# Optimization experiments

Measured on AMD Instinct MI355X. Metric: run time of the kernel, lower is better.

The kernel has to match this reference:

```python
import jax, jax.numpy as jnp
import numpy as np

B, S, H = 32, 2048, 1024

def setup_inputs() -> dict:
    key = jax.random.key(0)
    k1, k2, k3, k4 = jax.random.split(key, 4)
    encoded_states = jax.random.normal(k1, (B, S, H), dtype=jnp.float32)
    # exactly one formula token (label 2) per sample at position 0.
    raw = jax.random.randint(k2, (B, S), 0, 10)
    sr_label = jnp.where(raw < 2, raw, -100)
    sr_label = sr_label.at[:, 0].set(2)
    W1 = jax.random.normal(k3, (H, 2 * H), dtype=jnp.float32) * (1.0 / np.sqrt(2 * H))
    b1 = jnp.zeros((H,), dtype=jnp.float32)
    W2 = jax.random.normal(k4, (2, H), dtype=jnp.float32) * (1.0 / np.sqrt(H))
    b2 = jnp.zeros((2,), dtype=jnp.float32)
    return {"encoded_states": encoded_states, "sr_label": sr_label,
            "W1": W1, "b1": b1, "W2": W2, "b2": b2}

def reference(encoded_states, sr_label, W1, b1, W2, b2):
    dt = encoded_states.dtype
    header_mask = (sr_label >= 0) & (sr_label < 2)          # (b, s)
    formula_mask = (sr_label == 2).astype(dt)               # exactly one per row
    # gather the single formula embedding per sample via masked sum
    formula_emb = jnp.einsum('bs,bsh->bh', formula_mask, encoded_states)  # (b, h)
    fuse = jnp.concatenate(
        [encoded_states, jnp.broadcast_to(formula_emb[:, None, :], encoded_states.shape)],
        axis=-1)                                             # (b, s, 2h)
    hid = jax.nn.gelu(jnp.einsum('bsf,hf->bsh', fuse, W1) + b1, approximate=False)
    logits = jnp.einsum('bsh,ch->bsc', hid, W2) + b2         # (b, s, 2)
    logp = jax.nn.log_softmax(logits, axis=-1)
    labels = jnp.clip(sr_label, 0, 1)                        # safe index; masked below
    tok_loss = -jnp.take_along_axis(logp, labels[..., None], axis=-1)[..., 0]
    m = header_mask.astype(dt)
    cnt = m.sum(axis=1)                                      # valid headers per sample
    sample_loss = (tok_loss * m).sum(axis=1) / jnp.maximum(cnt, 1.0)  # CE mean per sample
    valid = (cnt > 0).astype(dt)
    loss = (sample_loss * valid).sum() / (valid.sum() + 1e-6)
    return loss, logits, header_mask
```

## Files before the change

### kernel.cpp

```cpp
#include <hip/hip_runtime.h>
#include <math.h>


typedef __bf16 bf16x8 __attribute__((ext_vector_type(8)));
typedef float f32x4 __attribute__((ext_vector_type(4)));

struct alignas(16) BF8 { __bf16 h[8]; };
struct alignas(8)  BF4 { __bf16 h[4]; };

typedef const __attribute__((address_space(1))) void glb_void;
typedef __attribute__((address_space(3))) void lds_void;

#define SEQ 2048
#define NB  32
#define HID 1024
#define MROWS (NB * SEQ)
#define NKT 16

__device__ __forceinline__ float gelu_bf(float x) {
    float z  = 0.70710678118f * x;
    float az = fabsf(z);
    float t  = __builtin_amdgcn_rcpf(fmaf(0.3275911f, az, 1.0f));
    float poly = fmaf(fmaf(fmaf(fmaf(1.061405429f, t, -1.453152027f), t,
                         1.421413741f), t, -0.284496736f), t, 0.254829592f) * t;
    float ex = __expf(-az * az);
    float er = copysignf(fmaf(-poly, ex, 1.0f), z);
    return 0.5f * x * (1.0f + er);
}

__global__ void sr_init_logits(float* __restrict__ logits, const float* __restrict__ b2) {
    int i = blockIdx.x * 256 + threadIdx.x;
    if (i < MROWS * 2) logits[i] = b2[i & 1];
}

__global__ void sr_conv_w1(const float* __restrict__ W1, __bf16* __restrict__ Bt) {
    int gid = blockIdx.x * 256 + threadIdx.x;
    int h = gid >> 8;
    int kb = (gid & 255) * 4;
    float4 v = *(const float4*)&W1[(size_t)h * 2048 + kb];
    BF4 o;
    o.h[0] = (__bf16)v.x; o.h[1] = (__bf16)v.y; o.h[2] = (__bf16)v.z; o.h[3] = (__bf16)v.w;
    *(BF4*)&Bt[(size_t)h * 1024 + kb] = o;
}

__global__ void sr_femb(const float* __restrict__ enc, const int* __restrict__ lab,
                        float* __restrict__ femb) {
    __shared__ int cnt;
    __shared__ int idl[64];
    int b = blockIdx.x;
    int tid = threadIdx.x;
    if (tid == 0) cnt = 0;
    __syncthreads();
    for (int s = tid; s < SEQ; s += 256)
        if (lab[b * SEQ + s] == 2) {
            int p = atomicAdd(&cnt, 1);
            if (p < 64) idl[p] = s;
        }
    __syncthreads();
    float4 a = {0.f, 0.f, 0.f, 0.f};
    int n = cnt < 64 ? cnt : 64;
    for (int i = 0; i < n; ++i) {
        float4 v = *(const float4*)&enc[((size_t)b * SEQ + idl[i]) * HID + tid * 4];
        a.x += v.x; a.y += v.y; a.z += v.z; a.w += v.w;
    }
    *(float4*)&femb[b * HID + tid * 4] = a;
}

__global__ void sr_fc(const float* __restrict__ femb, const float* __restrict__ W1,
                      const float* __restrict__ b1, float* __restrict__ fcout) {
    int gw = (blockIdx.x * 256 + threadIdx.x) >> 6;
    int lane = threadIdx.x & 63;
    for (int i = 0; i < 16; ++i) {
        int d = gw * 16 + i;
        int b = d >> 10, h = d & 1023;
        const float* fe = femb + b * HID;
        const float* wr = W1 + (size_t)h * 2048 + 1024;
        float p = 0.f;
        #pragma unroll
        for (int t = 0; t < 16; ++t) {
            int k = lane + t * 64;
            p += fe[k] * wr[k];
        }
        #pragma unroll
        for (int off = 32; off; off >>= 1) p += __shfl_down(p, off);
        if (lane == 0) fcout[d] = p + b1[h];
    }
}

__global__ __launch_bounds__(512, 2)
void sr_gemm11(const float* __restrict__ enc, const __bf16* __restrict__ Bt,
               const float* __restrict__ fc, const float* __restrict__ W2,
               float* __restrict__ partg) {
    __shared__ __align__(16) unsigned char smem[139264];
    __bf16* LAb = (__bf16*)smem;
    __bf16* LBb = (__bf16*)(smem + 65536);
    float*  red = (float*)smem;

    int bid = blockIdx.x;
    int lgc = (bid & 7) * 128 + (bid >> 3);
    int pm = lgc >> 2, pn = lgc & 3;
    const int row0 = pm * 256, col0 = pn * 256;

    int tid = threadIdx.x;
    int wid = tid >> 6, lane = tid & 63;
    int wr = wid >> 2, wc = wid & 3;
    int l15 = lane & 15, lq = lane >> 4;

    f32x4 acc[2][2][4][2] = {};
    float4 fa[4][2];

    #define LOAD_A(kt) do {                                                       \
        _Pragma("unroll")                                                         \
        for (int i = 0; i < 4; ++i) {                                             \
            int q = i * 512 + tid;                                                \
            int r = q >> 3, c = q & 7;                                            \
            int sc = (c ^ (r & 7)) * 8 + (kt) * 64;                               \
            const float* s0 = &enc[(size_t)(row0 + r) * HID + sc];                \
            fa[i][0] = *(const float4*)s0;                                        \
            fa[i][1] = *(const float4*)(s0 + 4);                                  \
        }                                                                         \
    } while (0)

    #define WRITE_A(buf) do {                                                     \
        _Pragma("unroll")                                                         \
        for (int i = 0; i < 4; ++i) {                                             \
            int q = i * 512 + tid;                                                \
            BF8 t;                                                                \
            t.h[0] = (__bf16)fa[i][0].x; t.h[1] = (__bf16)fa[i][0].y;             \
            t.h[2] = (__bf16)fa[i][0].z; t.h[3] = (__bf16)fa[i][0].w;             \
            t.h[4] = (__bf16)fa[i][1].x; t.h[5] = (__bf16)fa[i][1].y;             \
            t.h[6] = (__bf16)fa[i][1].z; t.h[7] = (__bf16)fa[i][1].w;             \
            *(BF8*)&LAb[(buf) * 16384 + q * 8] = t;                               \
        }                                                                         \
    } while (0)

    #define STAGE_B(buf, kt) do {                                                 \
        _Pragma("unroll")                                                         \
        for (int i = 0; i < 4; ++i) {                                             \
            int q = i * 512 + tid;                                                \
            int r = q >> 3, c = q & 7;                                            \
            int sc = (c ^ (r & 7)) * 8 + (kt) * 64;                               \
            __builtin_amdgcn_global_load_lds(                                     \
                (glb_void*)(Bt + (size_t)(col0 + r) * HID + sc),                  \
                (lds_void*)(LBb + (buf) * 16384 + q * 8), 16, 0, 0);              \
        }                                                                         \
    } while (0)

    LOAD_A(0);
    STAGE_B(0, 0);
    WRITE_A(0);
    __syncthreads();

    int cur = 0;
    for (int kt = 0; kt < NKT; ++kt) {
        if (kt + 1 < NKT) {
            LOAD_A(kt + 1);
            STAGE_B(cur ^ 1, kt + 1);
        }

        const __bf16* LAc = LAb + cur * 16384;
        const __bf16* LBc = LBb + cur * 16384;
        bf16x8 bfr[2][2][2];
        #pragma unroll
        for (int qb = 0; qb < 2; ++qb)
            #pragma unroll
            for (int n = 0; n < 2; ++n)
                #pragma unroll
                for (int kk = 0; kk < 2; ++kk) {
                    int r = qb * 128 + wc * 32 + n * 16 + l15;
                    bfr[qb][n][kk] = *(const bf16x8*)
                        &LBc[r * 64 + (((kk * 4 + lq) ^ (r & 7)) * 8)];
                }
        #pragma unroll
        for (int qa = 0; qa < 2; ++qa) {
            bf16x8 af[4][2];
            #pragma unroll
            for (int m = 0; m < 4; ++m)
                #pragma unroll
                for (int kk = 0; kk < 2; ++kk) {
                    int r = qa * 128 + wr * 64 + m * 16 + l15;
                    af[m][kk] = *(const bf16x8*)
                        &LAc[r * 64 + (((kk * 4 + lq) ^ (r & 7)) * 8)];
                }
            #pragma unroll
            for (int qb = 0; qb < 2; ++qb)
                #pragma unroll
                for (int m = 0; m < 4; ++m)
                    #pragma unroll
                    for (int n = 0; n < 2; ++n)
                        #pragma unroll
                        for (int kk = 0; kk < 2; ++kk)
                            acc[qa][qb][m][n] = __builtin_amdgcn_mfma_f32_16x16x32_bf16(
                                af[m][kk], bfr[qb][n][kk], acc[qa][qb][m][n], 0, 0, 0);
        }

        if (kt + 1 < NKT) WRITE_A(cur ^ 1);
        __syncthreads();
        cur ^= 1;
    }
    #undef LOAD_A
    #undef WRITE_A
    #undef STAGE_B

    int b = row0 >> 11;
    float fcv[2][2], w2a[2][2], w2b[2][2];
    #pragma unroll
    for (int qb = 0; qb < 2; ++qb)
        #pragma unroll
        for (int n = 0; n < 2; ++n) {
            int h = col0 + qb * 128 + wc * 32 + n * 16 + l15;
            fcv[qb][n] = fc[b * HID + h];
            w2a[qb][n] = W2[h];
            w2b[qb][n] = W2[HID + h];
        }
    int e = wc * 16 + l15;
    #pragma unroll
    for (int qa = 0; qa < 2; ++qa)
        #pragma unroll
        for (int m = 0; m < 4; ++m)
            #pragma unroll
            for (int j = 0; j < 4; ++j) {
                int rloc = qa * 128 + wr * 64 + m * 16 + lq * 4 + j;
                float p0 = 0.f, p1 = 0.f;
                #pragma unroll
                for (int qb = 0; qb < 2; ++qb)
                    #pragma unroll
                    for (int n = 0; n < 2; ++n) {
                        float g = gelu_bf(acc[qa][qb][m][n][j] + fcv[qb][n]);
                        p0 += g * w2a[qb][n];
                        p1 += g * w2b[qb][n];
                    }
                red[(rloc * 2 + 0) * 68 + e] = p0;
                red[(rloc * 2 + 1) * 68 + e] = p1;
            }
    __syncthreads();
    {
        const f32x4* rp = (const f32x4*)&red[tid * 68];
        f32x4 sv = {0.f, 0.f, 0.f, 0.f};
        #pragma unroll
        for (int i = 0; i < 16; ++i) sv += rp[i];
        float s = sv[0] + sv[1] + sv[2] + sv[3];
        int row = tid >> 1, c = tid & 1;
        partg[((size_t)pn * MROWS + row0 + row) * 2 + c] = s;
    }
}

__global__ __launch_bounds__(256, 2)
void sr_gemm_fused(const float* __restrict__ enc, const __bf16* __restrict__ Bt,
                   const float* __restrict__ fc, const float* __restrict__ W2,
                   float* __restrict__ logits) {
    __shared__ __bf16 As[128 * 64];
    __shared__ __bf16 Bs[128 * 64];

    int bid = blockIdx.x;
    int logical = (bid & 7) * 512 + (bid >> 3);
    int pm = logical >> 3;
    int pn = logical & 7;

    int tid = threadIdx.x;
    int wid = tid >> 6, lane = tid & 63;
    int wm = wid >> 1, wn = wid & 1;

    const int row0 = pm * 128;
    const int col0 = pn * 128;

    f32x4 acc[4][4] = {};

    for (int kt = 0; kt < 16; ++kt) {
        int k0 = kt * 64;
        #pragma unroll
        for (int i = 0; i < 4; ++i) {
            int q = i * 256 + tid;
            int r = q >> 3;
            int cb = (q & 7) * 8;
            const __bf16* src = Bt + (size_t)(col0 + r) * 1024 + k0 + cb;
            __builtin_amdgcn_global_load_lds((glb_void*)src, (lds_void*)&Bs[q * 8], 16, 0, 0);
        }
        #pragma unroll
        for (int pp = 0; pp < 4; ++pp) {
            int e = pp * 2048 + tid * 8;
            int r = e >> 6, c = e & 63;
            const float* src = enc + (size_t)(row0 + r) * 1024 + k0 + c;
            float4 f0 = *(const float4*)src;
            float4 f1 = *(const float4*)(src + 4);
            BF8 t;
            t.h[0] = (__bf16)f0.x; t.h[1] = (__bf16)f0.y;
            t.h[2] = (__bf16)f0.z; t.h[3] = (__bf16)f0.w;
            t.h[4] = (__bf16)f1.x; t.h[5] = (__bf16)f1.y;
            t.h[6] = (__bf16)f1.z; t.h[7] = (__bf16)f1.w;
            *(BF8*)&As[r * 64 + c] = t;
        }
        __syncthreads();
        int lrow = lane & 15;
        int ak = (lane >> 4) * 8;
        #pragma unroll
        for (int kk = 0; kk < 2; ++kk) {
            bf16x8 a[4], b[4];
            #pragma unroll
            for (int m = 0; m < 4; ++m)
                a[m] = *(const bf16x8*)&As[(wm * 64 + m * 16 + lrow) * 64 + kk * 32 + ak];
            #pragma unroll
            for (int n = 0; n < 4; ++n)
                b[n] = *(const bf16x8*)&Bs[(wn * 64 + n * 16 + lrow) * 64 + kk * 32 + ak];
            #pragma unroll
            for (int m = 0; m < 4; ++m)
                #pragma unroll
                for (int n = 0; n < 4; ++n)
                    acc[m][n] = __builtin_amdgcn_mfma_f32_16x16x32_bf16(a[m], b[n], acc[m][n], 0, 0, 0);
        }
        __syncthreads();
    }

    int bidx = row0 >> 11;
    float fcv[4], w2a[4], w2b[4];
    #pragma unroll
    for (int n = 0; n < 4; ++n) {
        int h = col0 + wn * 64 + n * 16 + (lane & 15);
        fcv[n] = fc[bidx * HID + h];
        w2a[n] = W2[h];
        w2b[n] = W2[HID + h];
    }
    #pragma unroll
    for (int m = 0; m < 4; ++m) {
        int rbase = row0 + wm * 64 + m * 16 + (lane >> 4) * 4;
        #pragma unroll
        for (int j = 0; j < 4; ++j) {
            float p0 = 0.f, p1 = 0.f;
            #pragma unroll
            for (int n = 0; n < 4; ++n) {
                float g = gelu_bf(acc[m][n][j] + fcv[n]);
                p0 += g * w2a[n];
                p1 += g * w2b[n];
            }
            #pragma unroll
            for (int off = 1; off < 16; off <<= 1) {
                p0 += __shfl_xor(p0, off);
                p1 += __shfl_xor(p1, off);
            }
            if ((lane & 15) == 0) {
                int rg = rbase + j;
                atomicAdd(&logits[rg * 2 + 0], p0);
                atomicAdd(&logits[rg * 2 + 1], p1);
            }
        }
    }
}

__global__ void sr_loss_pg(const int* __restrict__ lab, const float* __restrict__ partg,
                           const float* __restrict__ b2, float* __restrict__ logits,
                           float* __restrict__ mask_out, float* __restrict__ sl,
                           float* __restrict__ validv) {
    int b = blockIdx.x;
    int tid = threadIdx.x;
    float b20 = b2[0], b21 = b2[1];
    float lsum = 0.f; int lcnt = 0;
    for (int s = tid; s < SEQ; s += 256) {
        size_t row = (size_t)b * SEQ + s;
        float l0 = b20, l1 = b21;
        #pragma unroll
        for (int q = 0; q < 4; ++q) {
            l0 += partg[((size_t)q * MROWS + row) * 2 + 0];
            l1 += partg[((size_t)q * MROWS + row) * 2 + 1];
        }
        logits[row * 2 + 0] = l0;
        logits[row * 2 + 1] = l1;
        int l = lab[row];
        bool hdr = (l == 0) || (l == 1);
        mask_out[row] = hdr ? 1.0f : 0.0f;
        if (hdr) {
            float mx = fmaxf(l0, l1);
            float lse = mx + logf(expf(l0 - mx) + expf(l1 - mx));
            lsum += lse - (l == 0 ? l0 : l1);
            lcnt++;
        }
    }
    #pragma unroll
    for (int off = 32; off; off >>= 1) {
        lsum += __shfl_down(lsum, off);
        lcnt += __shfl_down(lcnt, off);
    }
    __shared__ float wsum[4];
    __shared__ int wcnt[4];
    int wid = tid >> 6, lane = tid & 63;
    if (lane == 0) { wsum[wid] = lsum; wcnt[wid] = lcnt; }
    __syncthreads();
    if (tid == 0) {
        float S = wsum[0] + wsum[1] + wsum[2] + wsum[3];
        int C = wcnt[0] + wcnt[1] + wcnt[2] + wcnt[3];
        sl[b] = (C > 0) ? S / (float)C : 0.0f;
        validv[b] = (C > 0) ? 1.0f : 0.0f;
    }
}

__global__ void sr_loss(const int* __restrict__ lab, const float* __restrict__ logits,
                        float* __restrict__ mask_out, float* __restrict__ sl,
                        float* __restrict__ validv) {
    int b = blockIdx.x;
    int tid = threadIdx.x;
    float lsum = 0.f; int lcnt = 0;
    for (int s = tid; s < SEQ; s += 256) {
        int l = lab[b * SEQ + s];
        bool hdr = (l == 0) || (l == 1);
        mask_out[b * SEQ + s] = hdr ? 1.0f : 0.0f;
        if (hdr) {
            float l0 = logits[(b * SEQ + s) * 2];
            float l1 = logits[(b * SEQ + s) * 2 + 1];
            float mx = fmaxf(l0, l1);
            float lse = mx + logf(expf(l0 - mx) + expf(l1 - mx));
            lsum += lse - (l == 0 ? l0 : l1);
            lcnt++;
        }
    }
    #pragma unroll
    for (int off = 32; off; off >>= 1) {
        lsum += __shfl_down(lsum, off);
        lcnt += __shfl_down(lcnt, off);
    }
    __shared__ float wsum[4];
    __shared__ int wcnt[4];
    int wid = tid >> 6, lane = tid & 63;
    if (lane == 0) { wsum[wid] = lsum; wcnt[wid] = lcnt; }
    __syncthreads();
    if (tid == 0) {
        float S = wsum[0] + wsum[1] + wsum[2] + wsum[3];
        int C = wcnt[0] + wcnt[1] + wcnt[2] + wcnt[3];
        sl[b] = (C > 0) ? S / (float)C : 0.0f;
        validv[b] = (C > 0) ? 1.0f : 0.0f;
    }
}

__global__ void sr_final(const float* __restrict__ sl, const float* __restrict__ validv,
                         float* __restrict__ out) {
    if (threadIdx.x == 0) {
        float s = 0.f, v = 0.f;
        for (int b = 0; b < NB; ++b) { s += sl[b]; v += validv[b]; }
        out[0] = s / (v + 1e-6f);
    }
}

extern "C" void kernel_launch(void* const* d_in, const int* in_sizes, int n_in,
                              void* d_out, int out_size, void* d_ws, size_t ws_size,
                              hipStream_t stream) {
    const float* enc = (const float*)d_in[0];
    const int*   lab = (const int*)d_in[1];
    const float* W1  = (const float*)d_in[2];
    const float* b1  = (const float*)d_in[3];
    const float* W2  = (const float*)d_in[4];
    const float* b2  = (const float*)d_in[5];

    float* out     = (float*)d_out;
    float* loss    = out;
    float* logits  = out + 1;
    float* maskout = out + 1 + MROWS * 2;

    float* ws     = (float*)d_ws;
    float* femb   = ws;
    float* fc     = ws + 32768;
    float* sl     = ws + 65536;
    float* validv = ws + 65568;
    float* partg  = ws + 65600;
    __bf16* Bt    = (__bf16*)(ws + 65600 + 2 * 524288);

    const size_t need = (65600u + 2u * 524288u) * 4u + (size_t)HID * HID * 2u;

    sr_conv_w1<<<1024, 256, 0, stream>>>(W1, Bt);
    sr_femb<<<32, 256, 0, stream>>>(enc, lab, femb);
    sr_fc<<<512, 256, 0, stream>>>(femb, W1, b1, fc);

    if (ws_size >= need) {
        sr_gemm11<<<1024, 512, 0, stream>>>(enc, Bt, fc, W2, partg);
        sr_loss_pg<<<32, 256, 0, stream>>>(lab, partg, b2, logits, maskout, sl, validv);
    } else {
        sr_init_logits<<<512, 256, 0, stream>>>(logits, b2);
        sr_gemm_fused<<<4096, 256, 0, stream>>>(enc, Bt, fc, W2, logits);
        sr_loss<<<32, 256, 0, stream>>>(lab, logits, maskout, sl, validv);
    }

    sr_final<<<1, 64, 0, stream>>>(sl, validv, loss);
}
```

Baseline: 263.2 us.

## Load A fragments directly to registers, giving each wave full tile width

The GEMM kernel no longer stages the fp32 activation tile through LDS as bf16. Each wave now loads its own 32 rows of A straight from global memory into registers, converts them to bf16 in place, and computes against all 256 columns of the B tile held in LDS. This removes the A shared-memory writes and reads and cuts LDS use from about 136KB to 64KB. In exchange each wave reads 16 B fragments from LDS per k-step with less reuse, and the A global loads use a less coalesced row-per-lane pattern. The cross-wave reduction buffer also shrinks.

Measured after the change: 279.6 us. 6.2% more time.

```diff
diff --git a/kernel.cpp b/kernel.cpp
--- a/kernel.cpp
+++ b/kernel.cpp
@@ -88,12 +88,11 @@
 }
 
 __global__ __launch_bounds__(512, 2)
-void sr_gemm11(const float* __restrict__ enc, const __bf16* __restrict__ Bt,
+void sr_gemm15(const float* __restrict__ enc, const __bf16* __restrict__ Bt,
                const float* __restrict__ fc, const float* __restrict__ W2,
                float* __restrict__ partg) {
-    __shared__ __align__(16) unsigned char smem[139264];
-    __bf16* LAb = (__bf16*)smem;
-    __bf16* LBb = (__bf16*)(smem + 65536);
+    __shared__ __align__(16) unsigned char smem[65536];
+    __bf16* LBb = (__bf16*)smem;
     float*  red = (float*)smem;
 
     int bid = blockIdx.x;
@@ -103,35 +102,40 @@
 
     int tid = threadIdx.x;
     int wid = tid >> 6, lane = tid & 63;
-    int wr = wid >> 2, wc = wid & 3;
     int l15 = lane & 15, lq = lane >> 4;
 
-    f32x4 acc[2][2][4][2] = {};
-    float4 fa[4][2];
+    f32x4 acc[2][16] = {};
+    float4 a32[2][2][2];
+    bf16x8 afb[2][2];
+
+    const float* arow0 = enc + (size_t)(row0 + wid * 32 + l15) * HID + lq * 8;
+    const float* arow1 = arow0 + 16 * HID;
 
     #define LOAD_A(kt) do {                                                       \
+        const float* s0 = arow0 + (kt) * 64;                                      \
+        const float* s1 = arow1 + (kt) * 64;                                      \
+        a32[0][0][0] = *(const float4*)s0;                                        \
+        a32[0][0][1] = *(const float4*)(s0 + 4);                                  \
+        a32[0][1][0] = *(const float4*)(s0 + 32);                                 \
+        a32[0][1][1] = *(const float4*)(s0 + 36);                                 \
+        a32[1][0][0] = *(const float4*)s1;                                        \
+        a32[1][0][1] = *(const float4*)(s1 + 4);                                  \
+        a32[1][1][0] = *(const float4*)(s1 + 32);                                 \
+        a32[1][1][1] = *(const float4*)(s1 + 36);                                 \
+    } while (0)
+
+    #define CVT_A() do {                                                          \
         _Pragma("unroll")                                                         \
-        for (int i = 0; i < 4; ++i) {                                             \
-            int q = i * 512 + tid;                                                \
-            int r = q >> 3, c = q & 7;                                            \
-            int sc = (c ^ (r & 7)) * 8 + (kt) * 64;                               \
-            const float* s0 = &enc[(size_t)(row0 + r) * HID + sc];                \
-            fa[i][0] = *(const float4*)s0;                                        \
-            fa[i][1] = *(const float4*)(s0 + 4);                                  \
-        }                                                                         \
-    } while (0)
-
-    #define WRITE_A(buf) do {                                                     \
-        _Pragma("unroll")                                                         \
-        for (int i = 0; i < 4; ++i) {                                             \
-            int q = i * 512 + tid;                                                \
-            BF8 t;                                                                \
-            t.h[0] = (__bf16)fa[i][0].x; t.h[1] = (__bf16)fa[i][0].y;             \
-            t.h[2] = (__bf16)fa[i][0].z; t.h[3] = (__bf16)fa[i][0].w;             \
-            t.h[4] = (__bf16)fa[i][1].x; t.h[5] = (__bf16)fa[i][1].y;             \
-            t.h[6] = (__bf16)fa[i][1].z; t.h[7] = (__bf16)fa[i][1].w;             \
-            *(BF8*)&LAb[(buf) * 16384 + q * 8] = t;                               \
-        }                                                                         \
+        for (int m = 0; m < 2; ++m)                                               \
+            _Pragma("unroll")                                                     \
+            for (int kk = 0; kk < 2; ++kk) {                                      \
+                BF8 t;                                                            \
+                t.h[0] = (__bf16)a32[m][kk][0].x; t.h[1] = (__bf16)a32[m][kk][0].y;\
+                t.h[2] = (__bf16)a32[m][kk][0].z; t.h[3] = (__bf16)a32[m][kk][0].w;\
+                t.h[4] = (__bf16)a32[m][kk][1].x; t.h[5] = (__bf16)a32[m][kk][1].y;\
+                t.h[6] = (__bf16)a32[m][kk][1].z; t.h[7] = (__bf16)a32[m][kk][1].w;\
+                afb[m][kk] = *(bf16x8*)&t;                                        \
+            }                                                                     \
     } while (0)
 
     #define STAGE_B(buf, kt) do {                                                 \
@@ -148,97 +152,64 @@
 
     LOAD_A(0);
     STAGE_B(0, 0);
-    WRITE_A(0);
     __syncthreads();
 
     int cur = 0;
     for (int kt = 0; kt < NKT; ++kt) {
-        if (kt + 1 < NKT) {
-            LOAD_A(kt + 1);
-            STAGE_B(cur ^ 1, kt + 1);
-        }
-
-        const __bf16* LAc = LAb + cur * 16384;
+        CVT_A();
+        int ktn = (kt + 1 < NKT) ? kt + 1 : NKT - 1;
+        LOAD_A(ktn);
+        if (kt + 1 < NKT) STAGE_B(cur ^ 1, kt + 1);
+
         const __bf16* LBc = LBb + cur * 16384;
-        bf16x8 bfr[2][2][2];
-        #pragma unroll
-        for (int qb = 0; qb < 2; ++qb)
-            #pragma unroll
-            for (int n = 0; n < 2; ++n)
-                #pragma unroll
-                for (int kk = 0; kk < 2; ++kk) {
-                    int r = qb * 128 + wc * 32 + n * 16 + l15;
-                    bfr[qb][n][kk] = *(const bf16x8*)
-                        &LBc[r * 64 + (((kk * 4 + lq) ^ (r & 7)) * 8)];
-                }
-        #pragma unroll
-        for (int qa = 0; qa < 2; ++qa) {
-            bf16x8 af[4][2];
-            #pragma unroll
-            for (int m = 0; m < 4; ++m)
-                #pragma unroll
-                for (int kk = 0; kk < 2; ++kk) {
-                    int r = qa * 128 + wr * 64 + m * 16 + l15;
-                    af[m][kk] = *(const bf16x8*)
-                        &LAc[r * 64 + (((kk * 4 + lq) ^ (r & 7)) * 8)];
-                }
-            #pragma unroll
-            for (int qb = 0; qb < 2; ++qb)
-                #pragma unroll
-                for (int m = 0; m < 4; ++m)
-                    #pragma unroll
-                    for (int n = 0; n < 2; ++n)
-                        #pragma unroll
-                        for (int kk = 0; kk < 2; ++kk)
-                            acc[qa][qb][m][n] = __builtin_amdgcn_mfma_f32_16x16x32_bf16(
-                                af[m][kk], bfr[qb][n][kk], acc[qa][qb][m][n], 0, 0, 0);
-        }
-
-        if (kt + 1 < NKT) WRITE_A(cur ^ 1);
+        #pragma unroll
+        for (int n = 0; n < 16; ++n) {
+            int r = n * 16 + l15;
+            bf16x8 b0 = *(const bf16x8*)&LBc[r * 64 + ((lq ^ (r & 7)) * 8)];
+            bf16x8 b1 = *(const bf16x8*)&LBc[r * 64 + (((4 + lq) ^ (r & 7)) * 8)];
+            #pragma unroll
+            for (int m = 0; m < 2; ++m) {
+                acc[m][n] = __builtin_amdgcn_mfma_f32_16x16x32_bf16(
+                    afb[m][0], b0, acc[m][n], 0, 0, 0);
+                acc[m][n] = __builtin_amdgcn_mfma_f32_16x16x32_bf16(
+                    afb[m][1], b1, acc[m][n], 0, 0, 0);
+            }
+        }
         __syncthreads();
         cur ^= 1;
     }
     #undef LOAD_A
-    #undef WRITE_A
+    #undef CVT_A
     #undef STAGE_B
 
     int b = row0 >> 11;
-    float fcv[2][2], w2a[2][2], w2b[2][2];
-    #pragma unroll
-    for (int qb = 0; qb < 2; ++qb)
-        #pragma unroll
-        for (int n = 0; n < 2; ++n) {
-            int h = col0 + qb * 128 + wc * 32 + n * 16 + l15;
-            fcv[qb][n] = fc[b * HID + h];
-            w2a[qb][n] = W2[h];
-            w2b[qb][n] = W2[HID + h];
-        }
-    int e = wc * 16 + l15;
-    #pragma unroll
-    for (int qa = 0; qa < 2; ++qa)
-        #pragma unroll
-        for (int m = 0; m < 4; ++m)
+    float p[2][4][2] = {};
+    #pragma unroll
+    for (int n = 0; n < 16; ++n) {
+        int h = col0 + n * 16 + l15;
+        float fcv = fc[b * HID + h];
+        float wa = W2[h], wb = W2[HID + h];
+        #pragma unroll
+        for (int m = 0; m < 2; ++m)
             #pragma unroll
             for (int j = 0; j < 4; ++j) {
-                int rloc = qa * 128 + wr * 64 + m * 16 + lq * 4 + j;
-                float p0 = 0.f, p1 = 0.f;
-                #pragma unroll
-                for (int qb = 0; qb < 2; ++qb)
-                    #pragma unroll
-                    for (int n = 0; n < 2; ++n) {
-                        float g = gelu_bf(acc[qa][qb][m][n][j] + fcv[qb][n]);
-                        p0 += g * w2a[qb][n];
-                        p1 += g * w2b[qb][n];
-                    }
-                red[(rloc * 2 + 0) * 68 + e] = p0;
-                red[(rloc * 2 + 1) * 68 + e] = p1;
+                float g = gelu_bf(acc[m][n][j] + fcv);
+                p[m][j][0] = fmaf(g, wa, p[m][j][0]);
+                p[m][j][1] = fmaf(g, wb, p[m][j][1]);
             }
+    }
+    #pragma unroll
+    for (int m = 0; m < 2; ++m)
+        #pragma unroll
+        for (int j = 0; j < 4; ++j) {
+            int rloc = wid * 32 + m * 16 + lq * 4 + j;
+            red[(rloc * 2 + 0) * 20 + l15] = p[m][j][0];
+            red[(rloc * 2 + 1) * 20 + l15] = p[m][j][1];
+        }
     __syncthreads();
     {
-        const f32x4* rp = (const f32x4*)&red[tid * 68];
-        f32x4 sv = {0.f, 0.f, 0.f, 0.f};
-        #pragma unroll
-        for (int i = 0; i < 16; ++i) sv += rp[i];
+        const f32x4* rp = (const f32x4*)&red[tid * 20];
+        f32x4 sv = rp[0] + rp[1] + rp[2] + rp[3];
         float s = sv[0] + sv[1] + sv[2] + sv[3];
         int row = tid >> 1, c = tid & 1;
         partg[((size_t)pn * MROWS + row0 + row) * 2 + c] = s;
@@ -468,7 +439,7 @@
     sr_fc<<<512, 256, 0, stream>>>(femb, W1, b1, fc);
 
     if (ws_size >= need) {
-        sr_gemm11<<<1024, 512, 0, stream>>>(enc, Bt, fc, W2, partg);
+        sr_gemm15<<<1024, 512, 0, stream>>>(enc, Bt, fc, W2, partg);
         sr_loss_pg<<<32, 256, 0, stream>>>(lab, partg, b2, logits, maskout, sl, validv);
     } else {
         sr_init_logits<<<512, 256, 0, stream>>>(logits, b2);
```
